# Optimization experiments

Measured on AMD Instinct MI355X. Metric: run time of the kernel, lower is better.

Reference implementation:

```python
import jax, jax.numpy as jnp
import numpy as np

N_UNITS = 1024
H = 8
D_K = N_UNITS // H
B, NCH, T = 4, 2, 1024


def setup_inputs() -> dict:
    key = jax.random.key(0)
    ks = jax.random.split(key, 9)
    s = 1.0 / np.sqrt(N_UNITS)
    inp = {
        "x": jax.random.normal(ks[0], (B, NCH, T, N_UNITS), dtype=jnp.float32),
        "batch_size": B,
        "Wq": jax.random.uniform(ks[1], (N_UNITS, N_UNITS), jnp.float32, -s, s),
        "bq": jax.random.uniform(ks[2], (N_UNITS,), jnp.float32, -s, s),
        "Wk": jax.random.uniform(ks[3], (N_UNITS, N_UNITS), jnp.float32, -s, s),
        "bk": jax.random.uniform(ks[4], (N_UNITS,), jnp.float32, -s, s),
        "Wv": jax.random.uniform(ks[5], (N_UNITS, N_UNITS), jnp.float32, -s, s),
        "bv": jax.random.uniform(ks[6], (N_UNITS,), jnp.float32, -s, s),
        "Wo": jax.random.uniform(ks[7], (N_UNITS, N_UNITS), jnp.float32, -s, s),
        "bo": jax.random.uniform(ks[8], (N_UNITS,), jnp.float32, -s, s),
    }
    return inp


def reference(x, batch_size, Wq, bq, Wk, bk, Wv, bv, Wo, bo):
    # x: [B, nch, T, n_units] (the 4D co-attention path)
    nch = x.shape[1]
    dk_co = D_K * nch  # _d_k in the original
    # Linear is y = x @ W.T + b
    q = jnp.einsum("bntu,vu->bntv", x, Wq) + bq  # [B,nch,T,U]
    k = jnp.einsum("bntu,vu->bntv", x, Wk) + bk
    v = jnp.einsum("bntu,vu->bntv", x, Wv) + bv
    # transpose(1,2) then reshape(B,-1,h,nch*d_k): [B,T,nch,U] -> [B,T,H,nch*d_k]
    q = jnp.transpose(q, (0, 2, 1, 3)).reshape(batch_size, -1, H, dk_co)
    k = jnp.transpose(k, (0, 2, 1, 3)).reshape(batch_size, -1, H, dk_co)
    # v: reshape(B, nch, -1, h, d_k) -> [B,nch,T,H,d_k]
    v = v.reshape(batch_size, nch, -1, H, D_K)
    # scores: [B,H,T,T], scaled by sqrt(nch*d_k)
    scores = jnp.einsum("bthd,bshd->bhts", q, k) / np.sqrt(dk_co)
    att = jax.nn.softmax(scores, axis=-1)  # dropout is identity in eval
    # expand of att across nch is implicit in the einsum (no materialized expand)
    out = jnp.einsum("bhts,bnshd->bnthd", att, v)  # [B,nch,T,H,d_k]
    out = out.reshape(batch_size, nch, -1, H * D_K)
    return jnp.einsum("bntu,vu->bntv", out, Wo) + bo
```

## Files before the change

kernel.cpp:

```cpp
#include <hip/hip_runtime.h>
#include <cstdint>
#include <cstddef>


typedef __bf16 bf16_t;
typedef __attribute__((ext_vector_type(8))) __bf16 bf16x8;
typedef __attribute__((ext_vector_type(4))) float f32x4;

__device__ __forceinline__ void async_copy16(const bf16_t* g, bf16_t* l) {
  auto* gp = reinterpret_cast<const __attribute__((address_space(1))) void*>(
      reinterpret_cast<uintptr_t>(g));
  auto* lp = reinterpret_cast<__attribute__((address_space(3))) void*>(
      reinterpret_cast<uintptr_t>(l));
  __builtin_amdgcn_global_load_lds(gp, lp, 16, 0, 0);
}

__global__ void cast_f32_bf16(const float* __restrict__ src,
                              bf16_t* __restrict__ dst, int n8) {
  int i = blockIdx.x * blockDim.x + threadIdx.x;
  if (i >= n8) return;
  const float4* s = (const float4*)src;
  float4 a = s[i * 2];
  float4 b = s[i * 2 + 1];
  bf16x8 o;
  o[0] = (bf16_t)a.x; o[1] = (bf16_t)a.y; o[2] = (bf16_t)a.z; o[3] = (bf16_t)a.w;
  o[4] = (bf16_t)b.x; o[5] = (bf16_t)b.y; o[6] = (bf16_t)b.z; o[7] = (bf16_t)b.w;
  *(bf16x8*)(dst + (size_t)i * 8) = o;
}

template <bool F32OUT>
__global__ __launch_bounds__(256, 2) void gemm_bt(
    const bf16_t* __restrict__ A, const bf16_t* __restrict__ W,
    const float* __restrict__ bias, void* __restrict__ Cout, int M, int N,
    int K, float scale) {
  __shared__ bf16_t sA[128 * 64];
  __shared__ bf16_t sB[128 * 64];
  const int tid = threadIdx.x;
  const int w = tid >> 6;
  const int lane = tid & 63;
  const int l15 = lane & 15;
  const int quad = lane >> 4;
  const int wm = (w >> 1) * 64;
  const int wn = (w & 1) * 64;
  const int m0 = blockIdx.x * 128;
  const int n0 = blockIdx.y * 128;

  const int srow = lane >> 3;
  const int sgrp = (lane & 7) ^ srow;
  const bf16_t* aB = A + (size_t)(m0 + srow) * K + sgrp * 8;
  const bf16_t* bB = W + (size_t)(n0 + srow) * K + sgrp * 8;

  f32x4 zero = {0.f, 0.f, 0.f, 0.f};
  f32x4 acc[4][4];
#pragma unroll
  for (int i = 0; i < 4; ++i)
#pragma unroll
    for (int j = 0; j < 4; ++j) acc[i][j] = zero;

  for (int kt = 0; kt < K; kt += 64) {
#pragma unroll
    for (int i = 0; i < 4; ++i) {
      const int c = w * 4 + i;
      async_copy16(aB + (size_t)(c * 8) * K + kt, &sA[c * 512]);
      async_copy16(bB + (size_t)(c * 8) * K + kt, &sB[c * 512]);
    }
    __syncthreads();
#pragma unroll
    for (int ks = 0; ks < 2; ++ks) {
      bf16x8 af[4], bfv[4];
#pragma unroll
      for (int mi = 0; mi < 4; ++mi) {
        const int row = wm + mi * 16 + l15;
        const int grp = ks * 4 + quad;
        af[mi] = *(const bf16x8*)&sA[row * 64 + ((grp ^ (row & 7)) << 3)];
      }
#pragma unroll
      for (int ni = 0; ni < 4; ++ni) {
        const int row = wn + ni * 16 + l15;
        const int grp = ks * 4 + quad;
        bfv[ni] = *(const bf16x8*)&sB[row * 64 + ((grp ^ (row & 7)) << 3)];
      }
#pragma unroll
      for (int mi = 0; mi < 4; ++mi)
#pragma unroll
        for (int ni = 0; ni < 4; ++ni)
          acc[mi][ni] = __builtin_amdgcn_mfma_f32_16x16x32_bf16(
              af[mi], bfv[ni], acc[mi][ni], 0, 0, 0);
    }
    __syncthreads();
  }

  float bv[4];
#pragma unroll
  for (int ni = 0; ni < 4; ++ni) bv[ni] = bias[n0 + wn + ni * 16 + l15];

#pragma unroll
  for (int mi = 0; mi < 4; ++mi) {
    const int rowb = m0 + wm + mi * 16 + quad * 4;
#pragma unroll
    for (int ni = 0; ni < 4; ++ni) {
      const int col = n0 + wn + ni * 16 + l15;
#pragma unroll
      for (int r = 0; r < 4; ++r) {
        const float v = (acc[mi][ni][r] + bv[ni]) * scale;
        if constexpr (F32OUT)
          ((float*)Cout)[(size_t)(rowb + r) * N + col] = v;
        else
          ((bf16_t*)Cout)[(size_t)(rowb + r) * N + col] = (bf16_t)v;
      }
    }
  }
}

__global__ void transpose_k(const bf16_t* __restrict__ src,
                            bf16_t* __restrict__ dst) {
  __shared__ bf16_t tile[64][72];
  const size_t zoff = (size_t)blockIdx.z * 1024 * 1024;
  const int r0 = blockIdx.x * 64;
  const int c0 = blockIdx.y * 64;
  const int t = threadIdx.x;
  const int lr = t >> 2;
  const int lc = (t & 3) * 16;
#pragma unroll
  for (int j = 0; j < 16; j += 8)
    *(bf16x8*)&tile[lr][lc + j] =
        *(const bf16x8*)&src[zoff + (size_t)(r0 + lr) * 1024 + c0 + lc + j];
  __syncthreads();
  bf16x8 o0, o1;
#pragma unroll
  for (int j = 0; j < 8; ++j) {
    o0[j] = tile[lc + j][lr];
    o1[j] = tile[lc + 8 + j][lr];
  }
  *(bf16x8*)&dst[zoff + (size_t)(c0 + lr) * 1024 + r0 + lc] = o0;
  *(bf16x8*)&dst[zoff + (size_t)(c0 + lr) * 1024 + r0 + lc + 8] = o1;
}

__global__ __launch_bounds__(256, 2) void attention_k(
    const bf16_t* __restrict__ qb, const bf16_t* __restrict__ kb,
    const bf16_t* __restrict__ vtb, bf16_t* __restrict__ ob) {
  __shared__ bf16_t sK[64 * 256];
  __shared__ bf16_t sV[256 * 64];
  __shared__ bf16_t sP[4][16 * 72];
  const int tid = threadIdx.x;
  const int w = tid >> 6;
  const int lane = tid & 63;
  const int l15 = lane & 15;
  const int quad = lane >> 4;
  const int qt = blockIdx.x, h = blockIdx.y, b = blockIdx.z;
  const int t0 = qt * 64;
  const size_t qkrow0 =
      ((size_t)(b * 2 + (h >> 2)) * 1024) * 1024 + (h & 3) * 256;

  bf16x8 qf[8];
  const bf16_t* qrow =
      qb + qkrow0 + (size_t)(t0 + w * 16 + l15) * 1024 + quad * 8;
#pragma unroll
  for (int kk = 0; kk < 8; ++kk) qf[kk] = *(const bf16x8*)(qrow + kk * 32);

  f32x4 o[16];
#pragma unroll
  for (int i = 0; i < 16; ++i) o[i] = (f32x4){0.f, 0.f, 0.f, 0.f};
  float m[4] = {-1e30f, -1e30f, -1e30f, -1e30f};
  float l[4] = {0.f, 0.f, 0.f, 0.f};

  const int krow_l = w * 2 + (lane >> 5);
  const int kslot = lane & 31;
  const int vrow_l = w * 8 + (lane >> 3);
  const int vslot = lane & 7;

  for (int st = 0; st < 16; ++st) {
#pragma unroll
    for (int r = 0; r < 8; ++r) {
      const int lr = r * 8 + krow_l;
      const int g = kslot ^ (lr & 7);
      async_copy16(kb + qkrow0 + (size_t)(st * 64 + lr) * 1024 + g * 8,
                   &sK[(r * 8 + w * 2) * 256]);
    }
#pragma unroll
    for (int r = 0; r < 8; ++r) {
      const int c = r * 32 + vrow_l;
      const int g = vslot ^ (c & 7);
      async_copy16(
          vtb + ((size_t)(b * 2 + (c >> 7)) * 1024 + h * 128 + (c & 127)) * 1024 +
              st * 64 + g * 8,
          &sV[(r * 32 + w * 8) * 64]);
    }
    __syncthreads();

    f32x4 s4[4];
#pragma unroll
    for (int nt = 0; nt < 4; ++nt) s4[nt] = (f32x4){0.f, 0.f, 0.f, 0.f};
#pragma unroll
    for (int kk = 0; kk < 8; ++kk) {
#pragma unroll
      for (int nt = 0; nt < 4; ++nt) {
        bf16x8 kf = *(const bf16x8*)&sK[(nt * 16 + l15) * 256 +
                                        (((kk * 4 + quad) ^ (l15 & 7)) << 3)];
        s4[nt] =
            __builtin_amdgcn_mfma_f32_16x16x32_bf16(qf[kk], kf, s4[nt], 0, 0, 0);
      }
    }

    float alpha[4];
    int changed = 0;
#pragma unroll
    for (int r = 0; r < 4; ++r) {
      float tm = fmaxf(fmaxf(s4[0][r], s4[1][r]), fmaxf(s4[2][r], s4[3][r]));
#pragma unroll
      for (int d = 1; d < 16; d <<= 1) tm = fmaxf(tm, __shfl_xor(tm, d, 64));
      const float mn = fmaxf(m[r], tm);
      alpha[r] = __builtin_amdgcn_exp2f(m[r] - mn);
      changed |= (mn > m[r]) ? 1 : 0;
      m[r] = mn;
      float ps = 0.f;
#pragma unroll
      for (int nt = 0; nt < 4; ++nt) {
        const float p = __builtin_amdgcn_exp2f(s4[nt][r] - mn);
        sP[w][(quad * 4 + r) * 72 + nt * 16 + l15] = (bf16_t)p;
        ps += p;
      }
#pragma unroll
      for (int d = 1; d < 16; d <<= 1) ps += __shfl_xor(ps, d, 64);
      l[r] = l[r] * alpha[r] + ps;
    }
    if (__any(changed)) {
#pragma unroll
      for (int ct = 0; ct < 16; ++ct)
#pragma unroll
        for (int r = 0; r < 4; ++r) o[ct][r] *= alpha[r];
    }
    asm volatile("s_waitcnt lgkmcnt(0)" ::: "memory");

#pragma unroll
    for (int kk = 0; kk < 2; ++kk) {
      bf16x8 pf = *(const bf16x8*)&sP[w][l15 * 72 + kk * 32 + quad * 8];
#pragma unroll
      for (int ct = 0; ct < 16; ++ct) {
        bf16x8 vf = *(const bf16x8*)&sV[(ct * 16 + l15) * 64 +
                                        (((kk * 4 + quad) ^ (l15 & 7)) << 3)];
        o[ct] = __builtin_amdgcn_mfma_f32_16x16x32_bf16(pf, vf, o[ct], 0, 0, 0);
      }
    }
    __syncthreads();
  }

  float rl[4];
#pragma unroll
  for (int r = 0; r < 4; ++r) rl[r] = 1.0f / l[r];
#pragma unroll
  for (int ct = 0; ct < 16; ++ct) {
    const int c = ct * 16 + l15;
    const int outc = h * 128 + (c & 127);
    const size_t rbase =
        ((size_t)(b * 2 + (c >> 7)) * 1024 + t0 + w * 16 + quad * 4) * 1024 +
        outc;
#pragma unroll
    for (int r = 0; r < 4; ++r)
      ob[rbase + (size_t)r * 1024] = (bf16_t)(o[ct][r] * rl[r]);
  }
}

extern "C" void kernel_launch(void* const* d_in, const int* in_sizes, int n_in,
                              void* d_out, int out_size, void* d_ws,
                              size_t ws_size, hipStream_t stream) {
  const float* x = (const float*)d_in[0];
  const float* Wq = (const float*)d_in[2];
  const float* bq = (const float*)d_in[3];
  const float* Wk = (const float*)d_in[4];
  const float* bk = (const float*)d_in[5];
  const float* Wv = (const float*)d_in[6];
  const float* bv = (const float*)d_in[7];
  const float* Wo = (const float*)d_in[8];
  const float* bo = (const float*)d_in[9];
  float* out = (float*)d_out;

  char* ws = (char*)d_ws;
  const size_t MB = 1u << 20;
  bf16_t* xb = (bf16_t*)(ws);
  bf16_t* qb = (bf16_t*)(ws + 16 * MB);
  bf16_t* kb = (bf16_t*)(ws + 32 * MB);
  bf16_t* vb = (bf16_t*)(ws + 48 * MB);
  bf16_t* vtb = (bf16_t*)(ws + 64 * MB);
  bf16_t* wqb = (bf16_t*)(ws + 80 * MB);
  bf16_t* wkb = (bf16_t*)(ws + 82 * MB);
  bf16_t* wvb = (bf16_t*)(ws + 84 * MB);
  bf16_t* wob = (bf16_t*)(ws + 86 * MB);
  bf16_t* ob = xb;

  cast_f32_bf16<<<4096, 256, 0, stream>>>(x, xb, 8 * 1024 * 1024 / 8);
  cast_f32_bf16<<<512, 256, 0, stream>>>(Wq, wqb, 1024 * 1024 / 8);
  cast_f32_bf16<<<512, 256, 0, stream>>>(Wk, wkb, 1024 * 1024 / 8);
  cast_f32_bf16<<<512, 256, 0, stream>>>(Wv, wvb, 1024 * 1024 / 8);
  cast_f32_bf16<<<512, 256, 0, stream>>>(Wo, wob, 1024 * 1024 / 8);

  dim3 gg(8192 / 128, 1024 / 128);
  gemm_bt<false><<<gg, 256, 0, stream>>>(xb, wqb, bq, qb, 8192, 1024, 1024,
                                         0.0625f * 1.4426950408889634f);
  gemm_bt<false><<<gg, 256, 0, stream>>>(xb, wkb, bk, kb, 8192, 1024, 1024,
                                         1.0f);
  gemm_bt<false><<<gg, 256, 0, stream>>>(xb, wvb, bv, vb, 8192, 1024, 1024,
                                         1.0f);

  transpose_k<<<dim3(16, 16, 8), 256, 0, stream>>>(vb, vtb);

  attention_k<<<dim3(16, 8, 4), 256, 0, stream>>>(qb, kb, vtb, ob);

  gemm_bt<true><<<gg, 256, 0, stream>>>(ob, wob, bo, out, 8192, 1024, 1024,
                                        1.0f);
}
```

Measured before the change: 269.7 us.

## Fuse casts and QKV GEMMs, write V transposed, double-buffer attention K/V tiles

The five cast launches become a single kernel, and the three Q/K/V projections run as one GEMM over a concatenated weight. The V slice's epilogue writes its output transposed directly, which removes the separate transpose kernel and its round trip through memory. The attention kernel now uses 32-key tiles with double-buffered async loads, so the next tile's fetch overlaps the current compute and one barrier per iteration is dropped. In exchange, the transposed V stores are narrow and strided, and the smaller tiles double the number of loop iterations.

Result: no change. 267.6 us (-0.8%).

```diff
diff --git a/kernel.cpp b/kernel.cpp
--- a/kernel.cpp
+++ b/kernel.cpp
@@ -5,6 +5,7 @@
 
 typedef __bf16 bf16_t;
 typedef __attribute__((ext_vector_type(8))) __bf16 bf16x8;
+typedef __attribute__((ext_vector_type(4))) __bf16 bf16x4;
 typedef __attribute__((ext_vector_type(4))) float f32x4;
 
 __device__ __forceinline__ void async_copy16(const bf16_t* g, bf16_t* l) {
@@ -15,24 +16,41 @@
   __builtin_amdgcn_global_load_lds(gp, lp, 16, 0, 0);
 }
 
-__global__ void cast_f32_bf16(const float* __restrict__ src,
-                              bf16_t* __restrict__ dst, int n8) {
-  int i = blockIdx.x * blockDim.x + threadIdx.x;
-  if (i >= n8) return;
-  const float4* s = (const float4*)src;
-  float4 a = s[i * 2];
-  float4 b = s[i * 2 + 1];
+__device__ __forceinline__ void cast8(const float* s, bf16_t* d) {
+  const float4 a = ((const float4*)s)[0];
+  const float4 b = ((const float4*)s)[1];
   bf16x8 o;
   o[0] = (bf16_t)a.x; o[1] = (bf16_t)a.y; o[2] = (bf16_t)a.z; o[3] = (bf16_t)a.w;
   o[4] = (bf16_t)b.x; o[5] = (bf16_t)b.y; o[6] = (bf16_t)b.z; o[7] = (bf16_t)b.w;
-  *(bf16x8*)(dst + (size_t)i * 8) = o;
-}
-
-template <bool F32OUT>
-__global__ __launch_bounds__(256, 2) void gemm_bt(
+  *(bf16x8*)d = o;
+}
+
+__global__ void cast_all(const float* __restrict__ x,
+                         const float* __restrict__ Wq,
+                         const float* __restrict__ Wk,
+                         const float* __restrict__ Wv,
+                         const float* __restrict__ Wo, bf16_t* __restrict__ xb,
+                         bf16_t* __restrict__ wqkv, bf16_t* __restrict__ wob) {
+  const int i = blockIdx.x * blockDim.x + threadIdx.x;
+  if (i < 1048576) {
+    cast8(x + (size_t)i * 8, xb + (size_t)i * 8);
+  } else {
+    const int j = i - 1048576;
+    if (j < 393216) {
+      const int seg = j >> 17;
+      const float* w = (seg == 0) ? Wq : ((seg == 1) ? Wk : Wv);
+      cast8(w + (size_t)(j - seg * 131072) * 8, wqkv + (size_t)j * 8);
+    } else if (j < 524288) {
+      cast8(Wo + (size_t)(j - 393216) * 8, wob + (size_t)(j - 393216) * 8);
+    }
+  }
+}
+
+__global__ __launch_bounds__(256, 2) void gemm_qkv(
     const bf16_t* __restrict__ A, const bf16_t* __restrict__ W,
-    const float* __restrict__ bias, void* __restrict__ Cout, int M, int N,
-    int K, float scale) {
+    const float* __restrict__ bq, const float* __restrict__ bk,
+    const float* __restrict__ bv, bf16_t* __restrict__ qb,
+    bf16_t* __restrict__ kb, bf16_t* __restrict__ vtb, float qscale) {
   __shared__ bf16_t sA[128 * 64];
   __shared__ bf16_t sB[128 * 64];
   const int tid = threadIdx.x;
@@ -44,18 +62,18 @@
   const int wn = (w & 1) * 64;
   const int m0 = blockIdx.x * 128;
   const int n0 = blockIdx.y * 128;
+  const int K = 1024;
 
   const int srow = lane >> 3;
   const int sgrp = (lane & 7) ^ srow;
   const bf16_t* aB = A + (size_t)(m0 + srow) * K + sgrp * 8;
   const bf16_t* bB = W + (size_t)(n0 + srow) * K + sgrp * 8;
 
-  f32x4 zero = {0.f, 0.f, 0.f, 0.f};
   f32x4 acc[4][4];
 #pragma unroll
   for (int i = 0; i < 4; ++i)
 #pragma unroll
-    for (int j = 0; j < 4; ++j) acc[i][j] = zero;
+    for (int j = 0; j < 4; ++j) acc[i][j] = (f32x4){0.f, 0.f, 0.f, 0.f};
 
   for (int kt = 0; kt < K; kt += 64) {
 #pragma unroll
@@ -90,10 +108,109 @@
     __syncthreads();
   }
 
-  float bv[4];
-#pragma unroll
-  for (int ni = 0; ni < 4; ++ni) bv[ni] = bias[n0 + wn + ni * 16 + l15];
-
+  const int seg = n0 >> 10;
+  const float scale = (seg == 0) ? qscale : 1.0f;
+  const float* bp = (seg == 0) ? bq : ((seg == 1) ? bk : bv);
+  float bvr[4];
+#pragma unroll
+  for (int ni = 0; ni < 4; ++ni)
+    bvr[ni] = bp[(n0 + wn + ni * 16 + l15) & 1023];
+
+  if (seg < 2) {
+    bf16_t* out = (seg == 0) ? qb : kb;
+#pragma unroll
+    for (int mi = 0; mi < 4; ++mi) {
+      const int rowb = m0 + wm + mi * 16 + quad * 4;
+#pragma unroll
+      for (int ni = 0; ni < 4; ++ni) {
+        const int col = (n0 + wn + ni * 16 + l15) & 1023;
+#pragma unroll
+        for (int r = 0; r < 4; ++r)
+          out[(size_t)(rowb + r) * 1024 + col] =
+              (bf16_t)((acc[mi][ni][r] + bvr[ni]) * scale);
+      }
+    }
+  } else {
+#pragma unroll
+    for (int mi = 0; mi < 4; ++mi) {
+      const int rowb = m0 + wm + mi * 16 + quad * 4;
+      const int bn = rowb >> 10;
+      const int t = rowb & 1023;
+#pragma unroll
+      for (int ni = 0; ni < 4; ++ni) {
+        const int u = (n0 + wn + ni * 16 + l15) & 1023;
+        bf16x4 v4;
+#pragma unroll
+        for (int r = 0; r < 4; ++r) v4[r] = (bf16_t)(acc[mi][ni][r] + bvr[ni]);
+        *(bf16x4*)&vtb[((size_t)(bn * 1024 + u)) * 1024 + t] = v4;
+      }
+    }
+  }
+}
+
+__global__ __launch_bounds__(256, 2) void gemm_out(
+    const bf16_t* __restrict__ A, const bf16_t* __restrict__ W,
+    const float* __restrict__ bias, float* __restrict__ Cout) {
+  __shared__ bf16_t sA[128 * 64];
+  __shared__ bf16_t sB[128 * 64];
+  const int tid = threadIdx.x;
+  const int w = tid >> 6;
+  const int lane = tid & 63;
+  const int l15 = lane & 15;
+  const int quad = lane >> 4;
+  const int wm = (w >> 1) * 64;
+  const int wn = (w & 1) * 64;
+  const int m0 = blockIdx.x * 128;
+  const int n0 = blockIdx.y * 128;
+  const int K = 1024, N = 1024;
+
+  const int srow = lane >> 3;
+  const int sgrp = (lane & 7) ^ srow;
+  const bf16_t* aB = A + (size_t)(m0 + srow) * K + sgrp * 8;
+  const bf16_t* bB = W + (size_t)(n0 + srow) * K + sgrp * 8;
+
+  f32x4 acc[4][4];
+#pragma unroll
+  for (int i = 0; i < 4; ++i)
+#pragma unroll
+    for (int j = 0; j < 4; ++j) acc[i][j] = (f32x4){0.f, 0.f, 0.f, 0.f};
+
+  for (int kt = 0; kt < K; kt += 64) {
+#pragma unroll
+    for (int i = 0; i < 4; ++i) {
+      const int c = w * 4 + i;
+      async_copy16(aB + (size_t)(c * 8) * K + kt, &sA[c * 512]);
+      async_copy16(bB + (size_t)(c * 8) * K + kt, &sB[c * 512]);
+    }
+    __syncthreads();
+#pragma unroll
+    for (int ks = 0; ks < 2; ++ks) {
+      bf16x8 af[4], bfv[4];
+#pragma unroll
+      for (int mi = 0; mi < 4; ++mi) {
+        const int row = wm + mi * 16 + l15;
+        const int grp = ks * 4 + quad;
+        af[mi] = *(const bf16x8*)&sA[row * 64 + ((grp ^ (row & 7)) << 3)];
+      }
+#pragma unroll
+      for (int ni = 0; ni < 4; ++ni) {
+        const int row = wn + ni * 16 + l15;
+        const int grp = ks * 4 + quad;
+        bfv[ni] = *(const bf16x8*)&sB[row * 64 + ((grp ^ (row & 7)) << 3)];
+      }
+#pragma unroll
+      for (int mi = 0; mi < 4; ++mi)
+#pragma unroll
+        for (int ni = 0; ni < 4; ++ni)
+          acc[mi][ni] = __builtin_amdgcn_mfma_f32_16x16x32_bf16(
+              af[mi], bfv[ni], acc[mi][ni], 0, 0, 0);
+    }
+    __syncthreads();
+  }
+
+  float bvr[4];
+#pragma unroll
+  for (int ni = 0; ni < 4; ++ni) bvr[ni] = bias[n0 + wn + ni * 16 + l15];
 #pragma unroll
   for (int mi = 0; mi < 4; ++mi) {
     const int rowb = m0 + wm + mi * 16 + quad * 4;
@@ -101,47 +218,18 @@
     for (int ni = 0; ni < 4; ++ni) {
       const int col = n0 + wn + ni * 16 + l15;
 #pragma unroll
-      for (int r = 0; r < 4; ++r) {
-        const float v = (acc[mi][ni][r] + bv[ni]) * scale;
-        if constexpr (F32OUT)
-          ((float*)Cout)[(size_t)(rowb + r) * N + col] = v;
-        else
-          ((bf16_t*)Cout)[(size_t)(rowb + r) * N + col] = (bf16_t)v;
-      }
-    }
-  }
-}
-
-__global__ void transpose_k(const bf16_t* __restrict__ src,
-                            bf16_t* __restrict__ dst) {
-  __shared__ bf16_t tile[64][72];
-  const size_t zoff = (size_t)blockIdx.z * 1024 * 1024;
-  const int r0 = blockIdx.x * 64;
-  const int c0 = blockIdx.y * 64;
-  const int t = threadIdx.x;
-  const int lr = t >> 2;
-  const int lc = (t & 3) * 16;
-#pragma unroll
-  for (int j = 0; j < 16; j += 8)
-    *(bf16x8*)&tile[lr][lc + j] =
-        *(const bf16x8*)&src[zoff + (size_t)(r0 + lr) * 1024 + c0 + lc + j];
-  __syncthreads();
-  bf16x8 o0, o1;
-#pragma unroll
-  for (int j = 0; j < 8; ++j) {
-    o0[j] = tile[lc + j][lr];
-    o1[j] = tile[lc + 8 + j][lr];
-  }
-  *(bf16x8*)&dst[zoff + (size_t)(c0 + lr) * 1024 + r0 + lc] = o0;
-  *(bf16x8*)&dst[zoff + (size_t)(c0 + lr) * 1024 + r0 + lc + 8] = o1;
+      for (int r = 0; r < 4; ++r)
+        Cout[(size_t)(rowb + r) * N + col] = acc[mi][ni][r] + bvr[ni];
+    }
+  }
 }
 
 __global__ __launch_bounds__(256, 2) void attention_k(
     const bf16_t* __restrict__ qb, const bf16_t* __restrict__ kb,
     const bf16_t* __restrict__ vtb, bf16_t* __restrict__ ob) {
-  __shared__ bf16_t sK[64 * 256];
-  __shared__ bf16_t sV[256 * 64];
-  __shared__ bf16_t sP[4][16 * 72];
+  __shared__ bf16_t sK[2][32 * 256];
+  __shared__ bf16_t sV[2][256 * 32];
+  __shared__ bf16_t sP[4][16 * 40];
   const int tid = threadIdx.x;
   const int w = tid >> 6;
   const int lane = tid & 63;
@@ -158,47 +246,59 @@
 #pragma unroll
   for (int kk = 0; kk < 8; ++kk) qf[kk] = *(const bf16x8*)(qrow + kk * 32);
 
+  const bf16_t* ksrc[4];
+  const bf16_t* vsrc[4];
+#pragma unroll
+  for (int i = 0; i < 4; ++i) {
+    const int p = w * 4 + i;
+    const int lr = p * 2 + (lane >> 5);
+    const int gk = (lane & 31) ^ (lr & 7);
+    ksrc[i] = kb + qkrow0 + (size_t)lr * 1024 + gk * 8;
+    const int c = p * 16 + (lane >> 2);
+    const int gv = (lane & 3) ^ ((c >> 1) & 3);
+    vsrc[i] = vtb + ((size_t)(b * 2 + (c >> 7)) * 1024 + h * 128 + (c & 127)) *
+                        1024 +
+              gv * 8;
+  }
+
   f32x4 o[16];
 #pragma unroll
   for (int i = 0; i < 16; ++i) o[i] = (f32x4){0.f, 0.f, 0.f, 0.f};
   float m[4] = {-1e30f, -1e30f, -1e30f, -1e30f};
   float l[4] = {0.f, 0.f, 0.f, 0.f};
 
-  const int krow_l = w * 2 + (lane >> 5);
-  const int kslot = lane & 31;
-  const int vrow_l = w * 8 + (lane >> 3);
-  const int vslot = lane & 7;
-
-  for (int st = 0; st < 16; ++st) {
-#pragma unroll
-    for (int r = 0; r < 8; ++r) {
-      const int lr = r * 8 + krow_l;
-      const int g = kslot ^ (lr & 7);
-      async_copy16(kb + qkrow0 + (size_t)(st * 64 + lr) * 1024 + g * 8,
-                   &sK[(r * 8 + w * 2) * 256]);
-    }
-#pragma unroll
-    for (int r = 0; r < 8; ++r) {
-      const int c = r * 32 + vrow_l;
-      const int g = vslot ^ (c & 7);
-      async_copy16(
-          vtb + ((size_t)(b * 2 + (c >> 7)) * 1024 + h * 128 + (c & 127)) * 1024 +
-              st * 64 + g * 8,
-          &sV[(r * 32 + w * 8) * 64]);
-    }
-    __syncthreads();
-
-    f32x4 s4[4];
-#pragma unroll
-    for (int nt = 0; nt < 4; ++nt) s4[nt] = (f32x4){0.f, 0.f, 0.f, 0.f};
+#pragma unroll
+  for (int i = 0; i < 4; ++i) {
+    async_copy16(ksrc[i], &sK[0][(w * 4 + i) * 512]);
+    async_copy16(vsrc[i], &sV[0][(w * 4 + i) * 512]);
+  }
+
+  for (int st = 0; st < 32; ++st) {
+    const int buf = st & 1;
+    __syncthreads();
+    if (st < 31) {
+      const int nb = buf ^ 1;
+#pragma unroll
+      for (int i = 0; i < 4; ++i) {
+        async_copy16(ksrc[i] + (size_t)(st + 1) * 32768,
+                     &sK[nb][(w * 4 + i) * 512]);
+        async_copy16(vsrc[i] + (size_t)(st + 1) * 32,
+                     &sV[nb][(w * 4 + i) * 512]);
+      }
+    }
+
+    f32x4 s4[2];
+    s4[0] = (f32x4){0.f, 0.f, 0.f, 0.f};
+    s4[1] = (f32x4){0.f, 0.f, 0.f, 0.f};
 #pragma unroll
     for (int kk = 0; kk < 8; ++kk) {
 #pragma unroll
-      for (int nt = 0; nt < 4; ++nt) {
-        bf16x8 kf = *(const bf16x8*)&sK[(nt * 16 + l15) * 256 +
-                                        (((kk * 4 + quad) ^ (l15 & 7)) << 3)];
-        s4[nt] =
-            __builtin_amdgcn_mfma_f32_16x16x32_bf16(qf[kk], kf, s4[nt], 0, 0, 0);
+      for (int nt = 0; nt < 2; ++nt) {
+        bf16x8 kf = *(const bf16x8*)&sK[buf][(nt * 16 + l15) * 256 +
+                                            (((kk * 4 + quad) ^ (l15 & 7))
+                                             << 3)];
+        s4[nt] = __builtin_amdgcn_mfma_f32_16x16x32_bf16(qf[kk], kf, s4[nt], 0,
+                                                         0, 0);
       }
     }
 
@@ -206,7 +306,7 @@
     int changed = 0;
 #pragma unroll
     for (int r = 0; r < 4; ++r) {
-      float tm = fmaxf(fmaxf(s4[0][r], s4[1][r]), fmaxf(s4[2][r], s4[3][r]));
+      float tm = fmaxf(s4[0][r], s4[1][r]);
 #pragma unroll
       for (int d = 1; d < 16; d <<= 1) tm = fmaxf(tm, __shfl_xor(tm, d, 64));
       const float mn = fmaxf(m[r], tm);
@@ -215,9 +315,9 @@
       m[r] = mn;
       float ps = 0.f;
 #pragma unroll
-      for (int nt = 0; nt < 4; ++nt) {
+      for (int nt = 0; nt < 2; ++nt) {
         const float p = __builtin_amdgcn_exp2f(s4[nt][r] - mn);
-        sP[w][(quad * 4 + r) * 72 + nt * 16 + l15] = (bf16_t)p;
+        sP[w][(quad * 4 + r) * 40 + nt * 16 + l15] = (bf16_t)p;
         ps += p;
       }
 #pragma unroll
@@ -232,17 +332,13 @@
     }
     asm volatile("s_waitcnt lgkmcnt(0)" ::: "memory");
 
-#pragma unroll
-    for (int kk = 0; kk < 2; ++kk) {
-      bf16x8 pf = *(const bf16x8*)&sP[w][l15 * 72 + kk * 32 + quad * 8];
-#pragma unroll
-      for (int ct = 0; ct < 16; ++ct) {
-        bf16x8 vf = *(const bf16x8*)&sV[(ct * 16 + l15) * 64 +
-                                        (((kk * 4 + quad) ^ (l15 & 7)) << 3)];
-        o[ct] = __builtin_amdgcn_mfma_f32_16x16x32_bf16(pf, vf, o[ct], 0, 0, 0);
-      }
-    }
-    __syncthreads();
+    bf16x8 pf = *(const bf16x8*)&sP[w][l15 * 40 + quad * 8];
+#pragma unroll
+    for (int ct = 0; ct < 16; ++ct) {
+      bf16x8 vf = *(const bf16x8*)&sV[buf][(ct * 16 + l15) * 32 +
+                                           ((quad ^ ((l15 >> 1) & 3)) << 3)];
+      o[ct] = __builtin_amdgcn_mfma_f32_16x16x32_bf16(pf, vf, o[ct], 0, 0, 0);
+    }
   }
 
   float rl[4];
@@ -280,32 +376,17 @@
   bf16_t* xb = (bf16_t*)(ws);
   bf16_t* qb = (bf16_t*)(ws + 16 * MB);
   bf16_t* kb = (bf16_t*)(ws + 32 * MB);
-  bf16_t* vb = (bf16_t*)(ws + 48 * MB);
-  bf16_t* vtb = (bf16_t*)(ws + 64 * MB);
-  bf16_t* wqb = (bf16_t*)(ws + 80 * MB);
-  bf16_t* wkb = (bf16_t*)(ws + 82 * MB);
-  bf16_t* wvb = (bf16_t*)(ws + 84 * MB);
-  bf16_t* wob = (bf16_t*)(ws + 86 * MB);
+  bf16_t* vtb = (bf16_t*)(ws + 48 * MB);
+  bf16_t* wqkv = (bf16_t*)(ws + 64 * MB);
+  bf16_t* wob = (bf16_t*)(ws + 70 * MB);
   bf16_t* ob = xb;
 
-  cast_f32_bf16<<<4096, 256, 0, stream>>>(x, xb, 8 * 1024 * 1024 / 8);
-  cast_f32_bf16<<<512, 256, 0, stream>>>(Wq, wqb, 1024 * 1024 / 8);
-  cast_f32_bf16<<<512, 256, 0, stream>>>(Wk, wkb, 1024 * 1024 / 8);
-  cast_f32_bf16<<<512, 256, 0, stream>>>(Wv, wvb, 1024 * 1024 / 8);
-  cast_f32_bf16<<<512, 256, 0, stream>>>(Wo, wob, 1024 * 1024 / 8);
-
-  dim3 gg(8192 / 128, 1024 / 128);
-  gemm_bt<false><<<gg, 256, 0, stream>>>(xb, wqb, bq, qb, 8192, 1024, 1024,
-                                         0.0625f * 1.4426950408889634f);
-  gemm_bt<false><<<gg, 256, 0, stream>>>(xb, wkb, bk, kb, 8192, 1024, 1024,
-                                         1.0f);
-  gemm_bt<false><<<gg, 256, 0, stream>>>(xb, wvb, bv, vb, 8192, 1024, 1024,
-                                         1.0f);
-
-  transpose_k<<<dim3(16, 16, 8), 256, 0, stream>>>(vb, vtb);
+  cast_all<<<6144, 256, 0, stream>>>(x, Wq, Wk, Wv, Wo, xb, wqkv, wob);
+
+  gemm_qkv<<<dim3(64, 24), 256, 0, stream>>>(
+      xb, wqkv, bq, bk, bv, qb, kb, vtb, 0.0625f * 1.4426950408889634f);
 
   attention_k<<<dim3(16, 8, 4), 256, 0, stream>>>(qb, kb, vtb, ob);
 
-  gemm_bt<true><<<gg, 256, 0, stream>>>(ob, wob, bo, out, 8192, 1024, 1024,
-                                        1.0f);
-}
+  gemm_out<<<dim3(64, 8), 256, 0, stream>>>(ob, wob, bo, out);
+}
```
